# Performance work log

Measured on AMD Instinct MI355X. Metric: run time of the kernel, lower is better.

## Reference

```python
import jax, jax.numpy as jnp
import numpy as np

B, N, E, H = 4, 2048, 768, 8
D = E // H
SCALING = D ** (-0.5)


def setup_inputs() -> dict:
    key = jax.random.key(0)
    k0, k1, k2, k3, k4 = jax.random.split(key, 5)
    x = jax.random.normal(k0, (B, N, E), dtype=jnp.float32)
    Wqkv = jax.random.normal(k1, (E, 3 * E), dtype=jnp.float32) * 0.02
    bqkv = jax.random.normal(k2, (3 * E,), dtype=jnp.float32) * 0.02
    Wproj = jax.random.normal(k3, (E, E), dtype=jnp.float32) * 0.02
    bproj = jax.random.normal(k4, (E,), dtype=jnp.float32) * 0.02
    return {"x": x, "Wqkv": Wqkv, "bqkv": bqkv, "Wproj": Wproj, "bproj": bproj}


def reference(x, Wqkv, bqkv, Wproj, bproj):
    b, n, e = x.shape
    h, d = H, E // H
    # QKV projection: [b, n, 3e]
    qkv = x @ Wqkv + bqkv
    # rearrange 'b n (h d qkv) -> qkv b h n d': qkv is the INNERMOST axis
    qkv = qkv.reshape(b, n, h, d, 3)
    q = jnp.transpose(qkv[..., 0], (0, 2, 1, 3))  # [b, h, n, d]
    k = jnp.transpose(qkv[..., 1], (0, 2, 1, 3))
    v = jnp.transpose(qkv[..., 2], (0, 2, 1, 3))
    # unscaled attention scores, softmax, then post-softmax scaling (as in source)
    energy = jnp.einsum('bhqd,bhkd->bhqk', q, k)  # [b, h, n, n]
    att = jax.nn.softmax(energy, axis=-1) * SCALING
    out = jnp.einsum('bhqk,bhkd->bhqd', att, v)   # [b, h, n, d]
    out = jnp.transpose(out, (0, 2, 1, 3)).reshape(b, n, e)
    return out @ Wproj + bproj
```

## Files before the change

kernel.cpp:

```cpp
#include <hip/hip_runtime.h>
#include <cstdint>

#define BB 4
#define SEQ 2048
#define EMB 768
#define NH 8
#define HD 96
#define E3 2304
#define MTOK 8192
#define SCALING 0.10206207261596575f
#define LOG2E 1.44269504f

typedef unsigned short u16;
typedef unsigned int u32;
typedef __bf16 bf16x8 __attribute__((ext_vector_type(8)));
typedef float f32x4 __attribute__((ext_vector_type(4)));
typedef float f32x16 __attribute__((ext_vector_type(16)));

__device__ __forceinline__ u16 f2bf(float f) {
    union { float f; uint32_t u; } c; c.f = f;
    uint32_t u = c.u;
    return (u16)((u + 0x7FFFu + ((u >> 16) & 1u)) >> 16);
}
__device__ __forceinline__ u16 f2bf_fast(float f) {
    union { float f; uint32_t u; } c; c.f = f;
    return (u16)((c.u + 0x8000u) >> 16);
}
__device__ __forceinline__ uint32_t pk2(float a, float b) {
    return (uint32_t)f2bf(a) | ((uint32_t)f2bf(b) << 16);
}
__device__ __forceinline__ uint32_t pk2_fast(float a, float b) {
    return (uint32_t)f2bf_fast(a) | ((uint32_t)f2bf_fast(b) << 16);
}
__device__ __forceinline__ float fexp2(float x) {
    return __builtin_amdgcn_exp2f(x);
}
__device__ __forceinline__ void async16(const u16* g, u16* l) {
    __builtin_amdgcn_global_load_lds(
        (const __attribute__((address_space(1))) void*)g,
        (__attribute__((address_space(3))) void*)l, 16, 0, 0);
}


__global__ void cvt_x_kernel(const float* __restrict__ src, u16* __restrict__ dst, int n8) {
    int i = blockIdx.x * blockDim.x + threadIdx.x;
    if (i >= n8) return;
    const float4* s4 = (const float4*)src;
    float4 a = s4[2 * i];
    float4 c = s4[2 * i + 1];
    uint4 o;
    o.x = pk2(a.x, a.y); o.y = pk2(a.z, a.w);
    o.z = pk2(c.x, c.y); o.w = pk2(c.z, c.w);
    ((uint4*)dst)[i] = o;
}

__global__ __launch_bounds__(256) void transpose_w_kernel(const float* __restrict__ src,
                                                          u16* __restrict__ dst,
                                                          int ncols, int perm) {
    __shared__ float T[64][65];
    int j0 = blockIdx.x * 64, k0 = blockIdx.y * 64;
    int tid = threadIdx.x;
#pragma unroll
    for (int it = 0; it < 16; ++it) {
        int lin = it * 256 + tid;
        int rr = lin >> 6, jj = lin & 63;
        int j = j0 + jj;
        int c = perm ? (((j % 768) / 96) * 288 + (j % 96) * 3 + (j / 768)) : j;
        T[rr][jj] = src[(k0 + rr) * ncols + c];
    }
    __syncthreads();
#pragma unroll
    for (int it = 0; it < 16; ++it) {
        int lin = it * 256 + tid;
        int jr = lin >> 6, kc = lin & 63;
        dst[(j0 + jr) * 768 + k0 + kc] = f2bf(T[kc][jr]);
    }
}

__global__ void cvt_bias_kernel(const float* __restrict__ bqkv, float* __restrict__ bp) {
    int j = blockIdx.x * blockDim.x + threadIdx.x;
    if (j < E3) {
        int s = j / 768, rr = j % 768, hh = rr / 96, dd = rr % 96;
        bp[j] = bqkv[hh * 288 + dd * 3 + s];
    }
}


__device__ __forceinline__ void gemm_tiles(const u16* __restrict__ A,
                                           const u16* __restrict__ Bt,
                                           int m0, int n0, int tid,
                                           u16* As, u16* Bs, f32x4 acc[4][4]) {
    const int lane = tid & 63;
    const int w = tid >> 6;
    const int l15 = lane & 15;
    const int quad = lane >> 4;
    const int wr = (w >> 1) * 64;
    const int wc = (w & 1) * 64;
    const int swz = l15 & 7;
    for (int kb = 0; kb < 768; kb += 64) {
#pragma unroll
        for (int it = 0; it < 4; ++it) {
            int base = (w * 4 + it) * 64;
            int lin = base + lane;
            int row = lin >> 3, cl = lin & 7;
            int cg = cl ^ (row & 7);
            async16(&A[(size_t)(m0 + row) * 768 + kb + cg * 8], &As[base * 8]);
            async16(&Bt[(size_t)(n0 + row) * 768 + kb + cg * 8], &Bs[base * 8]);
        }
        __syncthreads();
#pragma unroll
        for (int ks = 0; ks < 2; ++ks) {
            bf16x8 af[4], bfg[4];
#pragma unroll
            for (int fi = 0; fi < 4; ++fi)
                af[fi] = *(const bf16x8*)&As[(wr + fi * 16 + l15) * 64 + (((ks * 4 + quad) ^ swz) * 8)];
#pragma unroll
            for (int fj = 0; fj < 4; ++fj)
                bfg[fj] = *(const bf16x8*)&Bs[(wc + fj * 16 + l15) * 64 + (((ks * 4 + quad) ^ swz) * 8)];
#pragma unroll
            for (int fi = 0; fi < 4; ++fi)
#pragma unroll
                for (int fj = 0; fj < 4; ++fj)
                    acc[fi][fj] = __builtin_amdgcn_mfma_f32_16x16x32_bf16(af[fi], bfg[fj], acc[fi][fj], 0, 0, 0);
        }
        __syncthreads();
    }
}

__global__ __launch_bounds__(256) void gemm_qkv_kernel(const u16* __restrict__ A,
                                                       const u16* __restrict__ Bt,
                                                       const float* __restrict__ bias,
                                                       u16* __restrict__ qb,
                                                       u16* __restrict__ kg,
                                                       u16* __restrict__ vt) {
    __shared__ __align__(16) u16 As[128 * 64];
    __shared__ __align__(16) u16 Bs[128 * 64];
    int tid = threadIdx.x;
    int n0 = blockIdx.x * 128, m0 = blockIdx.y * 128;
    f32x4 acc[4][4] = {};
    gemm_tiles(A, Bt, m0, n0, tid, As, Bs, acc);
    int lane = tid & 63, w = tid >> 6, l15 = lane & 15, quad = lane >> 4;
    int wr = (w >> 1) * 64, wc = (w & 1) * 64;
#pragma unroll
    for (int fj = 0; fj < 4; ++fj) {
        int j = n0 + wc + fj * 16 + l15;
        int s = j / 768, rr = j % 768;
        int hh = rr / 96, dd = rr % 96;
        float bv = bias[j];
#pragma unroll
        for (int fi = 0; fi < 4; ++fi) {
#pragma unroll
            for (int r = 0; r < 4; ++r) {
                int m = m0 + wr + fi * 16 + quad * 4 + r;
                int b = m >> 11, n = m & 2047;
                int bh = b * NH + hh;
                float v = acc[fi][fj][r] + bv;
                if (s == 0) {
                    qb[((size_t)bh * SEQ + n) * HD + dd] = f2bf(v * LOG2E);
                } else if (s == 1) {
                    int cp = (dd >> 3) ^ (n & 7);
                    kg[((size_t)bh * SEQ + n) * 128 + cp * 8 + (dd & 7)] = f2bf(v);
                } else {
                    int kk = (n & ~63) | ((((n >> 3) ^ dd) & 7) << 3) | (n & 7);
                    vt[((size_t)bh * HD + dd) * SEQ + kk] = f2bf(v);
                }
            }
        }
    }
}

__global__ __launch_bounds__(256) void gemm_proj_kernel(const u16* __restrict__ A,
                                                        const u16* __restrict__ Bt,
                                                        const float* __restrict__ bias,
                                                        float* __restrict__ out) {
    __shared__ __align__(16) u16 As[128 * 64];
    __shared__ __align__(16) u16 Bs[128 * 64];
    int tid = threadIdx.x;
    int n0 = blockIdx.x * 128, m0 = blockIdx.y * 128;
    f32x4 acc[4][4] = {};
    gemm_tiles(A, Bt, m0, n0, tid, As, Bs, acc);
    int lane = tid & 63, w = tid >> 6, l15 = lane & 15, quad = lane >> 4;
    int wr = (w >> 1) * 64, wc = (w & 1) * 64;
#pragma unroll
    for (int fj = 0; fj < 4; ++fj) {
        int j = n0 + wc + fj * 16 + l15;
        float bv = bias[j];
#pragma unroll
        for (int fi = 0; fi < 4; ++fi) {
#pragma unroll
            for (int r = 0; r < 4; ++r) {
                int m = m0 + wr + fi * 16 + quad * 4 + r;
                out[(size_t)m * 768 + j] = acc[fi][fj][r] + bv;
            }
        }
    }
}

__global__ __launch_bounds__(256) void attn_kernel(const u16* __restrict__ Q,
                                                   const u16* __restrict__ Kg,
                                                   const u16* __restrict__ Vt,
                                                   u16* __restrict__ AO) {
    __shared__ __align__(16) u16 Ks[64 * 128];
    __shared__ __align__(16) u16 Vs[96 * 64];
    int tid = threadIdx.x;
    int lane = tid & 63, w = tid >> 6;
    int l31 = lane & 31, hf = lane >> 5;
    int swz = l31 & 7;
    int qt = blockIdx.x, bh = blockIdx.y;
    int b = bh >> 3, head = bh & 7;
    const u16* qp = Q + (size_t)bh * SEQ * HD;
    const u16* kgp = Kg + (size_t)bh * SEQ * 128;
    const u16* vtp = Vt + (size_t)bh * HD * SEQ;
    int q0 = qt * 128 + w * 32;

    bf16x8 aq[6];
#pragma unroll
    for (int dc = 0; dc < 6; ++dc)
        aq[dc] = *(const bf16x8*)&qp[(size_t)(q0 + l31) * HD + dc * 16 + hf * 8];

    f32x16 Ot[3] = {};
    float lp = 0.f;

    for (int kt = 0; kt < SEQ / 64; ++kt) {
        int k0 = kt * 64;
#pragma unroll
        for (int it = 0; it < 4; ++it) {
            int cw = w * 4 + it;
            const u16* g = kgp + (size_t)(k0 + cw * 4 + (lane >> 4)) * 128 + (lane & 15) * 8;
            async16(g, &Ks[cw * 512]);
        }
#pragma unroll
        for (int it = 0; it < 3; ++it) {
            int vw = w * 3 + it;
            const u16* g = vtp + (size_t)(vw * 8 + (lane >> 3)) * SEQ + k0 + (lane & 7) * 8;
            async16(g, &Vs[vw * 512]);
        }
        __syncthreads();

        f32x16 Sv[2] = {};
#pragma unroll
        for (int tau = 0; tau < 2; ++tau) {
#pragma unroll
            for (int dc = 0; dc < 6; ++dc) {
                bf16x8 ka = *(const bf16x8*)&Ks[(tau * 32 + l31) * 128 + (((2 * dc + hf) ^ swz) * 8)];
                Sv[tau] = __builtin_amdgcn_mfma_f32_32x32x16_bf16(ka, aq[dc], Sv[tau], 0, 0, 0);
            }
        }

        u32 pk[2][4][2];
#pragma unroll
        for (int tau = 0; tau < 2; ++tau)
#pragma unroll
            for (int g = 0; g < 4; ++g)
#pragma unroll
                for (int u = 0; u < 2; ++u) {
                    float p0 = fexp2(Sv[tau][g * 4 + 2 * u]);
                    float p1 = fexp2(Sv[tau][g * 4 + 2 * u + 1]);
                    lp += p0 + p1;
                    pk[tau][g][u] = pk2_fast(p0, p1);
                }
        u32 rv[2][2][2];
#pragma unroll
        for (int tau = 0; tau < 2; ++tau)
#pragma unroll
            for (int kc = 0; kc < 2; ++kc)
#pragma unroll
                for (int u = 0; u < 2; ++u) {
                    u32 send = hf ? pk[tau][2 * kc][u] : pk[tau][2 * kc + 1][u];
                    rv[tau][kc][u] = (u32)__shfl_xor((int)send, 32);
                }
#pragma unroll
        for (int tau = 0; tau < 2; ++tau) {
#pragma unroll
            for (int kc = 0; kc < 2; ++kc) {
                union { u32 u[4]; bf16x8 v; } pf;
                pf.u[0] = hf ? rv[tau][kc][0] : pk[tau][2 * kc][0];
                pf.u[1] = hf ? rv[tau][kc][1] : pk[tau][2 * kc][1];
                pf.u[2] = hf ? pk[tau][2 * kc + 1][0] : rv[tau][kc][0];
                pf.u[3] = hf ? pk[tau][2 * kc + 1][1] : rv[tau][kc][1];
#pragma unroll
                for (int t = 0; t < 3; ++t) {
                    bf16x8 va = *(const bf16x8*)&Vs[(t * 32 + l31) * 64 + (((4 * tau + 2 * kc + hf) ^ swz) * 8)];
                    Ot[t] = __builtin_amdgcn_mfma_f32_32x32x16_bf16(va, pf.v, Ot[t], 0, 0, 0);
                }
            }
        }
        __syncthreads();
    }

    float l = lp + __shfl_xor(lp, 32);
    float sc = SCALING / l;
    int n = q0 + l31;
    size_t rowbase = ((size_t)b * SEQ + n) * EMB + head * HD;
#pragma unroll
    for (int t = 0; t < 3; ++t) {
#pragma unroll
        for (int g = 0; g < 4; ++g) {
            int d0 = t * 32 + 8 * g + 4 * hf;
            uint2 val;
            val.x = pk2(Ot[t][g * 4 + 0] * sc, Ot[t][g * 4 + 1] * sc);
            val.y = pk2(Ot[t][g * 4 + 2] * sc, Ot[t][g * 4 + 3] * sc);
            *(uint2*)&AO[rowbase + d0] = val;
        }
    }
}


extern "C" void kernel_launch(void* const* d_in, const int* in_sizes, int n_in,
                              void* d_out, int out_size, void* d_ws, size_t ws_size,
                              hipStream_t stream) {
    const float* x     = (const float*)d_in[0];
    const float* Wqkv  = (const float*)d_in[1];
    const float* bqkv  = (const float*)d_in[2];
    const float* Wproj = (const float*)d_in[3];
    const float* bproj = (const float*)d_in[4];
    float* out = (float*)d_out;

    char* p = (char*)d_ws;
    u16*   xb    = (u16*)p;  p += (size_t)MTOK * EMB * 2;
    u16*   wqkvt = (u16*)p;  p += (size_t)E3 * EMB * 2;
    float* bqkvp = (float*)p; p += (size_t)E3 * 4;
    u16*   wpt   = (u16*)p;  p += (size_t)EMB * EMB * 2;
    u16*   qb    = (u16*)p;  p += (size_t)MTOK * EMB * 2;
    u16*   kg    = (u16*)p;  p += (size_t)BB * NH * SEQ * 128 * 2;
    u16*   vt    = (u16*)p;  p += (size_t)MTOK * EMB * 2;
    u16*   ao    = (u16*)p;  p += (size_t)MTOK * EMB * 2;

    cvt_x_kernel<<<MTOK * EMB / 8 / 256, 256, 0, stream>>>(x, xb, MTOK * EMB / 8);
    transpose_w_kernel<<<dim3(E3 / 64, EMB / 64), 256, 0, stream>>>(Wqkv, wqkvt, E3, 1);
    transpose_w_kernel<<<dim3(EMB / 64, EMB / 64), 256, 0, stream>>>(Wproj, wpt, EMB, 0);
    cvt_bias_kernel<<<E3 / 256, 256, 0, stream>>>(bqkv, bqkvp);
    gemm_qkv_kernel<<<dim3(E3 / 128, MTOK / 128), 256, 0, stream>>>(xb, wqkvt, bqkvp, qb, kg, vt);
    attn_kernel<<<dim3(SEQ / 128, BB * NH), 256, 0, stream>>>(qb, kg, vt, ao);
    gemm_proj_kernel<<<dim3(EMB / 128, MTOK / 128), 256, 0, stream>>>(ao, wpt, bproj, out);
}
```

Measured before the change: 250.0 us.

## Split V projection into transposed GEMM and double-buffer attention K/V tiles

The V part of the QKV projection moves to its own GEMM that computes V^T directly (weights as A, activations as B). This makes the transposed V stores contiguous along the sequence axis instead of scattered. The attention kernel now double-buffers its K and V shared-memory tiles, issuing async loads for the next tile while computing on the current one. The bias permutation kernel is dropped and the bias is indexed directly in the epilogue. The cost is twice the LDS per block, which may lower occupancy, and one extra kernel launch.

```diff
diff --git a/kernel.cpp b/kernel.cpp
--- a/kernel.cpp
+++ b/kernel.cpp
@@ -56,32 +56,27 @@
 
 __global__ __launch_bounds__(256) void transpose_w_kernel(const float* __restrict__ src,
                                                           u16* __restrict__ dst,
-                                                          int ncols, int perm) {
+                                                          int ncols, int mode) {
     __shared__ float T[64][65];
     int j0 = blockIdx.x * 64, k0 = blockIdx.y * 64;
     int tid = threadIdx.x;
 #pragma unroll
     for (int it = 0; it < 16; ++it) {
         int lin = it * 256 + tid;
-        int rr = lin >> 6, jj = lin & 63;
+        int rr2 = lin >> 6, jj = lin & 63;
         int j = j0 + jj;
-        int c = perm ? (((j % 768) / 96) * 288 + (j % 96) * 3 + (j / 768)) : j;
-        T[rr][jj] = src[(k0 + rr) * ncols + c];
+        int c;
+        if (mode == 0) c = j;
+        else if (mode == 1) { int s = j / 768, rr = j % 768; c = (rr / 96) * 288 + (rr % 96) * 3 + s; }
+        else { c = (j / 96) * 288 + (j % 96) * 3 + 2; }
+        T[rr2][jj] = src[(k0 + rr2) * ncols + c];
     }
     __syncthreads();
 #pragma unroll
     for (int it = 0; it < 16; ++it) {
         int lin = it * 256 + tid;
         int jr = lin >> 6, kc = lin & 63;
-        dst[(j0 + jr) * 768 + k0 + kc] = f2bf(T[kc][jr]);
-    }
-}
-
-__global__ void cvt_bias_kernel(const float* __restrict__ bqkv, float* __restrict__ bp) {
-    int j = blockIdx.x * blockDim.x + threadIdx.x;
-    if (j < E3) {
-        int s = j / 768, rr = j % 768, hh = rr / 96, dd = rr % 96;
-        bp[j] = bqkv[hh * 288 + dd * 3 + s];
+        dst[(size_t)(j0 + jr) * 768 + k0 + kc] = f2bf(T[kc][jr]);
     }
 }
 
@@ -127,12 +122,11 @@
     }
 }
 
-__global__ __launch_bounds__(256) void gemm_qkv_kernel(const u16* __restrict__ A,
-                                                       const u16* __restrict__ Bt,
-                                                       const float* __restrict__ bias,
-                                                       u16* __restrict__ qb,
-                                                       u16* __restrict__ kg,
-                                                       u16* __restrict__ vt) {
+__global__ __launch_bounds__(256) void gemm_qk_kernel(const u16* __restrict__ A,
+                                                      const u16* __restrict__ Bt,
+                                                      const float* __restrict__ bqkv,
+                                                      u16* __restrict__ qb,
+                                                      u16* __restrict__ kg) {
     __shared__ __align__(16) u16 As[128 * 64];
     __shared__ __align__(16) u16 Bs[128 * 64];
     int tid = threadIdx.x;
@@ -146,7 +140,7 @@
         int j = n0 + wc + fj * 16 + l15;
         int s = j / 768, rr = j % 768;
         int hh = rr / 96, dd = rr % 96;
-        float bv = bias[j];
+        float bv = bqkv[hh * 288 + dd * 3 + s];
 #pragma unroll
         for (int fi = 0; fi < 4; ++fi) {
 #pragma unroll
@@ -157,13 +151,49 @@
                 float v = acc[fi][fj][r] + bv;
                 if (s == 0) {
                     qb[((size_t)bh * SEQ + n) * HD + dd] = f2bf(v * LOG2E);
-                } else if (s == 1) {
+                } else {
                     int cp = (dd >> 3) ^ (n & 7);
                     kg[((size_t)bh * SEQ + n) * 128 + cp * 8 + (dd & 7)] = f2bf(v);
-                } else {
-                    int kk = (n & ~63) | ((((n >> 3) ^ dd) & 7) << 3) | (n & 7);
-                    vt[((size_t)bh * HD + dd) * SEQ + kk] = f2bf(v);
                 }
+            }
+        }
+    }
+}
+
+__global__ __launch_bounds__(256) void gemm_v_kernel(const u16* __restrict__ A,
+                                                     const u16* __restrict__ Bt,
+                                                     const float* __restrict__ bqkv,
+                                                     u16* __restrict__ vt) {
+    __shared__ __align__(16) u16 As[128 * 64];
+    __shared__ __align__(16) u16 Bs[128 * 64];
+    int tid = threadIdx.x;
+    int n0 = blockIdx.x * 128, m0 = blockIdx.y * 128;
+    f32x4 acc[4][4] = {};
+    gemm_tiles(A, Bt, m0, n0, tid, As, Bs, acc);
+    int lane = tid & 63, w = tid >> 6, l15 = lane & 15, quad = lane >> 4;
+    int wr = (w >> 1) * 64, wc = (w & 1) * 64;
+    float bvs[4][4]; int hhs[4][4], dds[4][4];
+#pragma unroll
+    for (int fi = 0; fi < 4; ++fi)
+#pragma unroll
+        for (int r = 0; r < 4; ++r) {
+            int m = m0 + wr + fi * 16 + quad * 4 + r;
+            int hh = m / 96, dd = m % 96;
+            hhs[fi][r] = hh; dds[fi][r] = dd;
+            bvs[fi][r] = bqkv[hh * 288 + dd * 3 + 2];
+        }
+#pragma unroll
+    for (int fj = 0; fj < 4; ++fj) {
+        int n = n0 + wc + fj * 16 + l15;
+        int b = n >> 11, nn = n & 2047;
+#pragma unroll
+        for (int fi = 0; fi < 4; ++fi) {
+#pragma unroll
+            for (int r = 0; r < 4; ++r) {
+                int dd = dds[fi][r];
+                int kk = (nn & ~63) | ((((nn >> 3) ^ dd) & 7) << 3) | (nn & 7);
+                vt[((size_t)(b * NH + hhs[fi][r]) * HD + dd) * SEQ + kk] =
+                    f2bf(acc[fi][fj][r] + bvs[fi][r]);
             }
         }
     }
@@ -200,8 +230,8 @@
                                                    const u16* __restrict__ Kg,
                                                    const u16* __restrict__ Vt,
                                                    u16* __restrict__ AO) {
-    __shared__ __align__(16) u16 Ks[64 * 128];
-    __shared__ __align__(16) u16 Vs[96 * 64];
+    __shared__ __align__(16) u16 Ks[2][64 * 128];
+    __shared__ __align__(16) u16 Vs[2][96 * 64];
     int tid = threadIdx.x;
     int lane = tid & 63, w = tid >> 6;
     int l31 = lane & 31, hf = lane >> 5;
@@ -221,28 +251,35 @@
     f32x16 Ot[3] = {};
     float lp = 0.f;
 
-    for (int kt = 0; kt < SEQ / 64; ++kt) {
+    auto stage = [&](int kt, int buf) {
         int k0 = kt * 64;
 #pragma unroll
         for (int it = 0; it < 4; ++it) {
             int cw = w * 4 + it;
-            const u16* g = kgp + (size_t)(k0 + cw * 4 + (lane >> 4)) * 128 + (lane & 15) * 8;
-            async16(g, &Ks[cw * 512]);
+            async16(kgp + (size_t)(k0 + cw * 4 + (lane >> 4)) * 128 + (lane & 15) * 8,
+                    &Ks[buf][cw * 512]);
         }
 #pragma unroll
         for (int it = 0; it < 3; ++it) {
             int vw = w * 3 + it;
-            const u16* g = vtp + (size_t)(vw * 8 + (lane >> 3)) * SEQ + k0 + (lane & 7) * 8;
-            async16(g, &Vs[vw * 512]);
-        }
-        __syncthreads();
+            async16(vtp + (size_t)(vw * 8 + (lane >> 3)) * SEQ + k0 + (lane & 7) * 8,
+                    &Vs[buf][vw * 512]);
+        }
+    };
+
+    stage(0, 0);
+    __syncthreads();
+
+    for (int kt = 0; kt < SEQ / 64; ++kt) {
+        int cur = kt & 1;
+        if (kt + 1 < SEQ / 64) stage(kt + 1, cur ^ 1);
 
         f32x16 Sv[2] = {};
 #pragma unroll
         for (int tau = 0; tau < 2; ++tau) {
 #pragma unroll
             for (int dc = 0; dc < 6; ++dc) {
-                bf16x8 ka = *(const bf16x8*)&Ks[(tau * 32 + l31) * 128 + (((2 * dc + hf) ^ swz) * 8)];
+                bf16x8 ka = *(const bf16x8*)&Ks[cur][(tau * 32 + l31) * 128 + (((2 * dc + hf) ^ swz) * 8)];
                 Sv[tau] = __builtin_amdgcn_mfma_f32_32x32x16_bf16(ka, aq[dc], Sv[tau], 0, 0, 0);
             }
         }
@@ -280,7 +317,7 @@
                 pf.u[3] = hf ? pk[tau][2 * kc + 1][1] : rv[tau][kc][1];
 #pragma unroll
                 for (int t = 0; t < 3; ++t) {
-                    bf16x8 va = *(const bf16x8*)&Vs[(t * 32 + l31) * 64 + (((4 * tau + 2 * kc + hf) ^ swz) * 8)];
+                    bf16x8 va = *(const bf16x8*)&Vs[cur][(t * 32 + l31) * 64 + (((4 * tau + 2 * kc + hf) ^ swz) * 8)];
                     Ot[t] = __builtin_amdgcn_mfma_f32_32x32x16_bf16(va, pf.v, Ot[t], 0, 0, 0);
                 }
             }
@@ -317,20 +354,21 @@
     float* out = (float*)d_out;
 
     char* p = (char*)d_ws;
-    u16*   xb    = (u16*)p;  p += (size_t)MTOK * EMB * 2;
-    u16*   wqkvt = (u16*)p;  p += (size_t)E3 * EMB * 2;
-    float* bqkvp = (float*)p; p += (size_t)E3 * 4;
-    u16*   wpt   = (u16*)p;  p += (size_t)EMB * EMB * 2;
-    u16*   qb    = (u16*)p;  p += (size_t)MTOK * EMB * 2;
-    u16*   kg    = (u16*)p;  p += (size_t)BB * NH * SEQ * 128 * 2;
-    u16*   vt    = (u16*)p;  p += (size_t)MTOK * EMB * 2;
-    u16*   ao    = (u16*)p;  p += (size_t)MTOK * EMB * 2;
+    u16*   xb   = (u16*)p;  p += (size_t)MTOK * EMB * 2;
+    u16*   wqkT = (u16*)p;  p += (size_t)1536 * EMB * 2;
+    u16*   wvr  = (u16*)p;  p += (size_t)EMB * EMB * 2;
+    u16*   wpt  = (u16*)p;  p += (size_t)EMB * EMB * 2;
+    u16*   qb   = (u16*)p;  p += (size_t)MTOK * EMB * 2;
+    u16*   kg   = (u16*)p;  p += (size_t)BB * NH * SEQ * 128 * 2;
+    u16*   vt   = (u16*)p;  p += (size_t)MTOK * EMB * 2;
+    u16*   ao   = (u16*)p;  p += (size_t)MTOK * EMB * 2;
 
     cvt_x_kernel<<<MTOK * EMB / 8 / 256, 256, 0, stream>>>(x, xb, MTOK * EMB / 8);
-    transpose_w_kernel<<<dim3(E3 / 64, EMB / 64), 256, 0, stream>>>(Wqkv, wqkvt, E3, 1);
+    transpose_w_kernel<<<dim3(1536 / 64, EMB / 64), 256, 0, stream>>>(Wqkv, wqkT, E3, 1);
+    transpose_w_kernel<<<dim3(EMB / 64, EMB / 64), 256, 0, stream>>>(Wqkv, wvr, E3, 2);
     transpose_w_kernel<<<dim3(EMB / 64, EMB / 64), 256, 0, stream>>>(Wproj, wpt, EMB, 0);
-    cvt_bias_kernel<<<E3 / 256, 256, 0, stream>>>(bqkv, bqkvp);
-    gemm_qkv_kernel<<<dim3(E3 / 128, MTOK / 128), 256, 0, stream>>>(xb, wqkvt, bqkvp, qb, kg, vt);
+    gemm_qk_kernel<<<dim3(1536 / 128, MTOK / 128), 256, 0, stream>>>(xb, wqkT, bqkv, qb, kg);
+    gemm_v_kernel<<<dim3(MTOK / 128, EMB / 128), 256, 0, stream>>>(wvr, xb, bqkv, vt);
     attn_kernel<<<dim3(SEQ / 128, BB * NH), 256, 0, stream>>>(qb, kg, vt, ao);
     gemm_proj_kernel<<<dim3(EMB / 128, MTOK / 128), 256, 0, stream>>>(ao, wpt, bproj, out);
 }
```

Result: slower. 255.5 us (+2.2%).
